# Kernel tuning notes

Measured on AMD Instinct MI355X. Metric: run time of the kernel, lower is better.

Reference implementation:

```python
import jax, jax.numpy as jnp
import numpy as np


def setup_inputs() -> dict:
    key = jax.random.key(0)
    k_cb, k_mask, k_y, k_yt, k_ym = jax.random.split(key, 5)
    B, L, M = 8, 2048, 4096
    CB = jax.random.normal(k_cb, (B, L, 3), dtype=jnp.float32) * 10.0
    # residue validity mask: mostly valid, some padding
    mask = (jax.random.uniform(k_mask, (B, L)) > 0.1).astype(jnp.float32)
    Y = jax.random.normal(k_y, (B, M, 3), dtype=jnp.float32) * 10.0
    Y_t = jax.random.randint(k_yt, (B, M), 0, 64, dtype=jnp.int32)
    Y_m = jax.random.randint(k_ym, (B, M), 0, 2, dtype=jnp.int32)
    return {"CB": CB, "mask": mask, "Y": Y, "Y_t": Y_t, "Y_m": Y_m,
            "number_of_ligand_atoms": 25}


def reference(CB, mask, Y, Y_t, Y_m, number_of_ligand_atoms):
    # CB: [B, L, 3], mask: [B, L], Y: [B, M, 3], Y_t/Y_m: [B, M]
    B, L, _ = CB.shape
    k = number_of_ligand_atoms
    Y_m_f = Y_m.astype(jnp.float32)
    mask_CBY = mask[:, :, None] * Y_m_f[:, None, :]          # [B, L, M]
    d = CB[:, :, None, :] - Y[:, None, :, :]                 # [B, L, M, 3]
    L2_AB = jnp.sum(d * d, axis=-1)                          # [B, L, M]
    L2_AB = L2_AB * mask_CBY + (1.0 - mask_CBY) * 1000.0
    # k smallest distances per (b, l); torch uses full argsort + slice,
    # top_k of the negated matrix selects the same set.
    neg_vals, nn_idx = jax.lax.top_k(-L2_AB, k)              # [B, L, k]
    L2_AB_nn = -neg_vals
    D_AB_closest = jnp.sqrt(L2_AB_nn[:, :, 0])               # [B, L]
    b_idx = jnp.arange(B)[:, None, None]                     # [B, 1, 1]
    Y_out = Y[b_idx, nn_idx]                                 # [B, L, k, 3]
    Y_t_out = Y_t[b_idx, nn_idx].astype(jnp.int32)           # [B, L, k]
    Y_m_out = Y_m[b_idx, nn_idx].astype(jnp.int32)           # [B, L, k]
    return Y_out, Y_t_out, Y_m_out, D_AB_closest
```

## Files before the change

### kernel.cpp

```cpp
#include <hip/hip_runtime.h>

#pragma clang fp contract(off)

typedef unsigned long long u64;
typedef unsigned int u32;
typedef unsigned short u16;
typedef float f32x2 __attribute__((ext_vector_type(2)));

#define BB 8
#define LL 2048
#define MM 4096
#define KK 25
#define WPB 16
#define TPB 1024
#define CAP 3072
#define SENT  0xFFFFFFFFFFFFFFFFull
#define SENTH 0xFFFFFFFFu

static __device__ __forceinline__ u32 wave_min_u32(u32 x) {
    u32 t;
    t = (u32)__builtin_amdgcn_update_dpp(0, (int)x, 0xB1, 0xF, 0xF, true);
    x = t < x ? t : x;
    t = (u32)__builtin_amdgcn_update_dpp(0, (int)x, 0x4E, 0xF, 0xF, true);
    x = t < x ? t : x;
    t = (u32)__builtin_amdgcn_update_dpp(0, (int)x, 0x141, 0xF, 0xF, true);
    x = t < x ? t : x;
    t = (u32)__builtin_amdgcn_update_dpp(0, (int)x, 0x140, 0xF, 0xF, true);
    x = t < x ? t : x;
    t = (u32)__builtin_amdgcn_update_dpp((int)x, (int)x, 0x142, 0xF, 0xF, false);
    x = t < x ? t : x;
    t = (u32)__builtin_amdgcn_update_dpp((int)x, (int)x, 0x143, 0xF, 0xF, false);
    x = t < x ? t : x;
    return (u32)__builtin_amdgcn_readlane((int)x, 63);
}

__global__ void __launch_bounds__(TPB, 8) knn_kernel(
    const float* __restrict__ CB, const float* __restrict__ maskA,
    const float* __restrict__ Y, const int* __restrict__ Yt,
    const int* __restrict__ Ym, float* __restrict__ out)
{
    __shared__ __align__(16) float sX[CAP];
    __shared__ __align__(16) float sY[CAP];
    __shared__ __align__(16) float sZ[CAP];
    __shared__ u16 sP16[CAP];
    __shared__ u16 sMidx[64];
    __shared__ int sWinc[16];
    __shared__ int sWbase[16];
    __shared__ int sVtot;
    __shared__ u32 sWinV[WPB][KK];
    __shared__ u16 sWinS[WPB][KK];

    const int tid  = threadIdx.x;
    const int lane = tid & 63;
    const int wv   = tid >> 6;
    const int blk  = blockIdx.x;
    const int b    = blk >> 7;
    const int qg   = blk & 127;

    const float* Yb  = Y  + (size_t)b * MM * 3;
    const int*   Ymb = Ym + (size_t)b * MM;
    const int*   Ytb = Yt + (size_t)b * MM;

    const int p0 = tid << 2;
    const float4 f0 = *(const float4*)(Yb + 3 * p0);
    const float4 f1 = *(const float4*)(Yb + 3 * p0 + 4);
    const float4 f2 = *(const float4*)(Yb + 3 * p0 + 8);
    const int4   m4 = *(const int4*)(Ymb + p0);
    const int v0 = (m4.x != 0), v1 = (m4.y != 0), v2 = (m4.z != 0), v3 = (m4.w != 0);
    const int cnt = v0 + v1 + v2 + v3;

    int inc = cnt;
#pragma unroll
    for (int off = 1; off < 64; off <<= 1) {
        const int t = __shfl_up(inc, off, 64);
        if (lane >= off) inc += t;
    }
    if (lane == 63) sWinc[wv] = inc;
    __syncthreads();
    if (tid < 16) {
        const int x = sWinc[tid];
        int ix = x;
#pragma unroll
        for (int off = 1; off < 16; off <<= 1) {
            const int t = __shfl_up(ix, off, 16);
            if (tid >= off) ix += t;
        }
        sWbase[tid] = ix - x;
        if (tid == 15) sVtot = ix;
    }
    __syncthreads();

    {
        int bs = sWbase[wv] + inc - cnt;
        int mb = p0 - bs;
        if (v0) { sX[bs]=f0.x; sY[bs]=f0.y; sZ[bs]=f0.z; sP16[bs]=(u16)(p0+0); bs++; }
        else    { if (mb < 64) sMidx[mb] = (u16)(p0 + 0); mb++; }
        if (v1) { sX[bs]=f0.w; sY[bs]=f1.x; sZ[bs]=f1.y; sP16[bs]=(u16)(p0+1); bs++; }
        else    { if (mb < 64) sMidx[mb] = (u16)(p0 + 1); mb++; }
        if (v2) { sX[bs]=f1.z; sY[bs]=f1.w; sZ[bs]=f2.x; sP16[bs]=(u16)(p0+2); bs++; }
        else    { if (mb < 64) sMidx[mb] = (u16)(p0 + 2); mb++; }
        if (v3) { sX[bs]=f2.y; sY[bs]=f2.z; sZ[bs]=f2.w; sP16[bs]=(u16)(p0+3); bs++; }
        else    { if (mb < 64) sMidx[mb] = (u16)(p0 + 3); mb++; }
    }
    const int V  = sVtot;
    const int NJ = (V + 127) >> 7;
    for (int c = V + tid; c < (NJ << 7); c += TPB) {
        sX[c] = __builtin_inff(); sY[c] = 0.0f; sZ[c] = 0.0f; sP16[c] = 4095;
    }
    __syncthreads();

    const int l = qg * WPB + wv;
    const int q = b * LL + l;

    float* out_y = out;
    float* out_t = out + (size_t)BB * LL * KK * 3;
    float* out_m = out_t + (size_t)BB * LL * KK;
    float* out_d = out_m + (size_t)BB * LL * KK;

    if (maskA[q] == 0.0f) {
        if (lane < KK) {
            const int p = lane;
            const size_t o = (size_t)q * KK + lane;
            out_y[3 * o + 0] = Yb[3 * p + 0];
            out_y[3 * o + 1] = Yb[3 * p + 1];
            out_y[3 * o + 2] = Yb[3 * p + 2];
            out_t[o] = (float)Ytb[p];
            out_m[o] = (float)Ymb[p];
            if (lane == 0) out_d[q] = sqrtf(1000.0f);
        }
        return;
    }

    const float cx = CB[3 * q + 0];
    const float cy = CB[3 * q + 1];
    const float cz = CB[3 * q + 2];

    float v1f = 3.0e38f, v2f = 3.0e38f, v3f = 3.0e38f, v4f = 3.0e38f;
    u32 J = 0u;
    const u32 SEL1 = 0x06050400u;
    const u32 SEL2 = 0x06050004u;
    const u32 SEL3 = 0x06000504u;
    const u32 SEL4 = 0x00060504u;
    auto ins = [&](float v, u32 id) {
        const bool c1 = v < v1f, c2 = v < v2f, c3 = v < v3f, c4 = v < v4f;
        const u32 sel = c1 ? SEL1 : (c2 ? SEL2 : (c3 ? SEL3 : SEL4));
        const u32 Jp  = __builtin_amdgcn_perm(J, id, sel);
        const float n2 = __builtin_amdgcn_fmed3f(v, v1f, v2f);
        const float n3 = __builtin_amdgcn_fmed3f(v, v2f, v3f);
        const float n4 = __builtin_amdgcn_fmed3f(v, v3f, v4f);
        v1f = fminf(v, v1f);
        v2f = n2; v3f = n3; v4f = n4;
        J = c4 ? Jp : J;
    };

    const f32x2 cxx = {cx, cx}, cyy = {cy, cy}, czz = {cz, cz};
#pragma unroll 4
    for (int j = 0; j < NJ; ++j) {
        const int base = (j << 7) + (lane << 1);
        const f32x2 xp = *(const f32x2*)&sX[base];
        const f32x2 yp = *(const f32x2*)&sY[base];
        const f32x2 zp = *(const f32x2*)&sZ[base];
        const f32x2 dx = cxx - xp;
        const f32x2 dy = cyy - yp;
        const f32x2 dz = czz - zp;
        const f32x2 dsq = (dx * dx + dy * dy) + dz * dz;
        ins(dsq.x, (u32)(j << 1));
        ins(dsq.y, (u32)((j << 1) | 1));
    }

    auto slotof = [&](u32 id) -> u32 {
        return ((id >> 1) << 7) | (u32)(lane << 1) | (id & 1u);
    };

    u32 h1 = __float_as_uint(v1f) + 1u;
    u32 h2 = __float_as_uint(v2f) + 1u;
    u32 h3 = __float_as_uint(v3f) + 1u;
    u32 h4 = __float_as_uint(v4f) + 1u;
    u64 lref = ((u64)h4 << 32) | slotof((J >> 24) & 0xFFu);

#pragma unroll 1
    for (int it = 0; it < KK; ++it) {
        if (it >= 4 && __any(h1 == SENTH)) {
            const bool need = (h1 == SENTH);
            u64 found = SENT;
            const int NI = NJ << 1;
#pragma unroll 4
            for (int id = 0; id < NI; ++id) {
                const u32 s = slotof((u32)id);
                const float dx = cx - sX[s];
                const float dy = cy - sY[s];
                const float dz = cz - sZ[s];
                const float v = (dx * dx + dy * dy) + dz * dz;
                const u64 key = ((u64)(__float_as_uint(v) + 1u) << 32) | s;
                if (key > lref && key < found) found = key;
            }
            if (need) {
                const u32 s = (u32)found & 0xFFFFu;
                h1 = (u32)(found >> 32);
                J = (J & ~0xFFu) | (((s >> 7) << 1) | (s & 1u));
                lref = found;
            }
        }
        const u32 bv = wave_min_u32(h1);
        const u64 ball = __ballot(h1 == bv);
        bool win = (h1 == bv);
        if (__popcll(ball) != 1) {
            const u32 vl = slotof(J & 0xFFu);
            u32 cp = win ? vl : 0xFFFFFFFFu;
#pragma unroll
            for (int off = 32; off; off >>= 1) {
                const u32 o = __shfl_xor(cp, off, 64);
                cp = (o < cp) ? o : cp;
            }
            win = win && (vl == cp);
        }
        if (win) {
            sWinV[wv][it] = h1;
            sWinS[wv][it] = (u16)slotof(J & 0xFFu);
            h1 = h2; h2 = h3; h3 = h4; h4 = SENTH;
            J >>= 8;
        }
    }

    u32 mvh = 0; u32 mslot = 0;
    if (lane < KK) { mvh = sWinV[wv][lane]; mslot = sWinS[wv][lane]; }
    const bool less = (lane < KK) && (mvh < 0x447A0001u);
    const int nless = __popcll(__ballot(less));
    if (lane < KK) {
        int p; float val, mflag;
        if (lane < nless) {
            p = (int)sP16[mslot];
            val = __uint_as_float(mvh - 1u);
            mflag = 1.0f;
        } else {
            p = (int)sMidx[lane - nless];
            val = 1000.0f;
            mflag = 0.0f;
        }
        const size_t o = (size_t)q * KK + lane;
        out_y[3 * o + 0] = Yb[3 * p + 0];
        out_y[3 * o + 1] = Yb[3 * p + 1];
        out_y[3 * o + 2] = Yb[3 * p + 2];
        out_t[o] = (float)Ytb[p];
        out_m[o] = mflag;
        if (lane == 0) out_d[q] = sqrtf(val);
    }
}

extern "C" void kernel_launch(void* const* d_in, const int* in_sizes, int n_in,
                              void* d_out, int out_size, void* d_ws, size_t ws_size,
                              hipStream_t stream) {
    const float* CB   = (const float*)d_in[0];
    const float* mask = (const float*)d_in[1];
    const float* Y    = (const float*)d_in[2];
    const int*   Yt   = (const int*)d_in[3];
    const int*   Ym   = (const int*)d_in[4];
    float* out = (float*)d_out;

    dim3 grid(BB * LL / WPB);
    dim3 block(TPB);
    hipLaunchKernelGGL(knn_kernel, grid, block, 0, stream, CB, mask, Y, Yt, Ym, out);
}
```

Baseline: 105.4 us.

## Replace serial 25-round wave-min extraction with bitonic-sort threshold selection

Instead of running 25 sequential wave-wide min reductions to pick the k nearest candidates, the kernel bitonic-sorts each lane's best value across the wave to get a threshold, compacts all per-lane candidates at or below it into shared memory, and bitonic-sorts those 64 keys to read off the top 25 directly. A validity check (candidate count exceeding 64, or some lane's 4-deep list possibly being exhausted before the 25th key) falls back to the original iterative path. This is meant to cut the long serial chain of reductions and shuffles per query. In exchange it adds two full 64-lane sorting networks, one of them on 64-bit keys, plus a prefix scan and extra shared memory traffic.

```diff
diff --git a/kernel.cpp b/kernel.cpp
--- a/kernel.cpp
+++ b/kernel.cpp
@@ -32,6 +32,38 @@
     t = (u32)__builtin_amdgcn_update_dpp((int)x, (int)x, 0x143, 0xF, 0xF, false);
     x = t < x ? t : x;
     return (u32)__builtin_amdgcn_readlane((int)x, 63);
+}
+
+static __device__ __forceinline__ u32 sort64_u32(u32 key, int lane) {
+#pragma unroll
+    for (int k = 2; k <= 64; k <<= 1) {
+#pragma unroll
+        for (int j = k >> 1; j >= 1; j >>= 1) {
+            const u32 o = (u32)__shfl_xor((int)key, j, 64);
+            const bool takeMin = ((lane & k) == 0) == ((lane & j) == 0);
+            const u32 mn = o < key ? o : key;
+            const u32 mx = o < key ? key : o;
+            key = takeMin ? mn : mx;
+        }
+    }
+    return key;
+}
+
+static __device__ __forceinline__ u64 sort64_u64(u64 key, int lane) {
+#pragma unroll
+    for (int k = 2; k <= 64; k <<= 1) {
+#pragma unroll
+        for (int j = k >> 1; j >= 1; j >>= 1) {
+            const u32 olo = (u32)__shfl_xor((int)(u32)key, j, 64);
+            const u32 ohi = (u32)__shfl_xor((int)(u32)(key >> 32), j, 64);
+            const u64 o = ((u64)ohi << 32) | olo;
+            const bool takeMin = ((lane & k) == 0) == ((lane & j) == 0);
+            const u64 mn = o < key ? o : key;
+            const u64 mx = o < key ? key : o;
+            key = takeMin ? mn : mx;
+        }
+    }
+    return key;
 }
 
 __global__ void __launch_bounds__(TPB, 8) knn_kernel(
@@ -47,8 +79,7 @@
     __shared__ int sWinc[16];
     __shared__ int sWbase[16];
     __shared__ int sVtot;
-    __shared__ u32 sWinV[WPB][KK];
-    __shared__ u16 sWinS[WPB][KK];
+    __shared__ u64 sExt[WPB][64];
 
     const int tid  = threadIdx.x;
     const int lane = tid & 63;
@@ -67,9 +98,9 @@
     const float4 f2 = *(const float4*)(Yb + 3 * p0 + 8);
     const int4   m4 = *(const int4*)(Ymb + p0);
     const int v0 = (m4.x != 0), v1 = (m4.y != 0), v2 = (m4.z != 0), v3 = (m4.w != 0);
-    const int cnt = v0 + v1 + v2 + v3;
-
-    int inc = cnt;
+    const int cnt0 = v0 + v1 + v2 + v3;
+
+    int inc = cnt0;
 #pragma unroll
     for (int off = 1; off < 64; off <<= 1) {
         const int t = __shfl_up(inc, off, 64);
@@ -91,7 +122,7 @@
     __syncthreads();
 
     {
-        int bs = sWbase[wv] + inc - cnt;
+        int bs = sWbase[wv] + inc - cnt0;
         int mb = p0 - bs;
         if (v0) { sX[bs]=f0.x; sY[bs]=f0.y; sZ[bs]=f0.z; sP16[bs]=(u16)(p0+0); bs++; }
         else    { if (mb < 64) sMidx[mb] = (u16)(p0 + 0); mb++; }
@@ -172,58 +203,95 @@
         return ((id >> 1) << 7) | (u32)(lane << 1) | (id & 1u);
     };
 
+    const u32 s1 = slotof( J        & 0xFFu);
+    const u32 s2 = slotof((J >>  8) & 0xFFu);
+    const u32 s3 = slotof((J >> 16) & 0xFFu);
+    const u32 s4 = slotof((J >> 24) & 0xFFu);
     u32 h1 = __float_as_uint(v1f) + 1u;
     u32 h2 = __float_as_uint(v2f) + 1u;
     u32 h3 = __float_as_uint(v3f) + 1u;
     u32 h4 = __float_as_uint(v4f) + 1u;
-    u64 lref = ((u64)h4 << 32) | slotof((J >> 24) & 0xFFu);
-
+    u64 lref = ((u64)h4 << 32) | s4;
+
+    bool fb = false;
+    u64 myk = 0;
+    {
+        const u32 T = (u32)__builtin_amdgcn_readlane((int)sort64_u32(h1, lane), 24);
+        const int c1 = (h1 <= T), c2 = (h2 <= T), c3 = (h3 <= T), c4 = (h4 <= T);
+        const int cnt = c1 + c2 + c3 + c4;
+        int incl = cnt;
+#pragma unroll
+        for (int off = 1; off < 64; off <<= 1) {
+            const int t = __shfl_up(incl, off, 64);
+            if (lane >= off) incl += t;
+        }
+        const int total = __builtin_amdgcn_readlane(incl, 63);
+        if (total > 64) {
+            fb = true;
+        } else {
+            u64* sE = sExt[wv];
+            sE[lane] = SENT;
+            int pos = incl - cnt;
+            if (c1) { sE[pos] = ((u64)h1 << 32) | s1; pos++; }
+            if (c2) { sE[pos] = ((u64)h2 << 32) | s2; pos++; }
+            if (c3) { sE[pos] = ((u64)h3 << 32) | s3; pos++; }
+            if (c4) { sE[pos] = ((u64)h4 << 32) | s4; pos++; }
+            myk = sort64_u64(sE[lane], lane);
+            const u32 k25lo = (u32)__builtin_amdgcn_readlane((int)(u32)myk, 24);
+            const u32 k25hi = (u32)__builtin_amdgcn_readlane((int)(u32)(myk >> 32), 24);
+            const u64 K25 = ((u64)k25hi << 32) | k25lo;
+            if (__any(lref < K25)) fb = true;
+        }
+    }
+
+    if (fb) {
 #pragma unroll 1
-    for (int it = 0; it < KK; ++it) {
-        if (it >= 4 && __any(h1 == SENTH)) {
-            const bool need = (h1 == SENTH);
-            u64 found = SENT;
-            const int NI = NJ << 1;
+        for (int it = 0; it < KK; ++it) {
+            if (it >= 4 && __any(h1 == SENTH)) {
+                const bool need = (h1 == SENTH);
+                u64 found = SENT;
+                const int NI = NJ << 1;
 #pragma unroll 4
-            for (int id = 0; id < NI; ++id) {
-                const u32 s = slotof((u32)id);
-                const float dx = cx - sX[s];
-                const float dy = cy - sY[s];
-                const float dz = cz - sZ[s];
-                const float v = (dx * dx + dy * dy) + dz * dz;
-                const u64 key = ((u64)(__float_as_uint(v) + 1u) << 32) | s;
-                if (key > lref && key < found) found = key;
+                for (int id = 0; id < NI; ++id) {
+                    const u32 s = slotof((u32)id);
+                    const float dx = cx - sX[s];
+                    const float dy = cy - sY[s];
+                    const float dz = cz - sZ[s];
+                    const float v = (dx * dx + dy * dy) + dz * dz;
+                    const u64 key = ((u64)(__float_as_uint(v) + 1u) << 32) | s;
+                    if (key > lref && key < found) found = key;
+                }
+                if (need) {
+                    const u32 s = (u32)found & 0xFFFFu;
+                    h1 = (u32)(found >> 32);
+                    J = (J & ~0xFFu) | (((s >> 7) << 1) | (s & 1u));
+                    lref = found;
+                }
             }
-            if (need) {
-                const u32 s = (u32)found & 0xFFFFu;
-                h1 = (u32)(found >> 32);
-                J = (J & ~0xFFu) | (((s >> 7) << 1) | (s & 1u));
-                lref = found;
+            const u32 bv = wave_min_u32(h1);
+            const u64 ball = __ballot(h1 == bv);
+            bool win = (h1 == bv);
+            if (__popcll(ball) != 1) {
+                const u32 vl = slotof(J & 0xFFu);
+                u32 cp = win ? vl : 0xFFFFFFFFu;
+#pragma unroll
+                for (int off = 32; off; off >>= 1) {
+                    const u32 o = __shfl_xor(cp, off, 64);
+                    cp = (o < cp) ? o : cp;
+                }
+                win = win && (vl == cp);
             }
-        }
-        const u32 bv = wave_min_u32(h1);
-        const u64 ball = __ballot(h1 == bv);
-        bool win = (h1 == bv);
-        if (__popcll(ball) != 1) {
-            const u32 vl = slotof(J & 0xFFu);
-            u32 cp = win ? vl : 0xFFFFFFFFu;
-#pragma unroll
-            for (int off = 32; off; off >>= 1) {
-                const u32 o = __shfl_xor(cp, off, 64);
-                cp = (o < cp) ? o : cp;
+            if (win) {
+                sExt[wv][it] = ((u64)h1 << 32) | slotof(J & 0xFFu);
+                h1 = h2; h2 = h3; h3 = h4; h4 = SENTH;
+                J >>= 8;
             }
-            win = win && (vl == cp);
-        }
-        if (win) {
-            sWinV[wv][it] = h1;
-            sWinS[wv][it] = (u16)slotof(J & 0xFFu);
-            h1 = h2; h2 = h3; h3 = h4; h4 = SENTH;
-            J >>= 8;
-        }
-    }
-
-    u32 mvh = 0; u32 mslot = 0;
-    if (lane < KK) { mvh = sWinV[wv][lane]; mslot = sWinS[wv][lane]; }
+        }
+        if (lane < KK) myk = sExt[wv][lane];
+    }
+
+    const u32 mvh   = (u32)(myk >> 32);
+    const u32 mslot = (u32)myk & 0xFFFFu;
     const bool less = (lane < KK) && (mvh < 0x447A0001u);
     const int nless = __popcll(__ballot(less));
     if (lane < KK) {
```

New measurement: 107.6 us. 1.02x slower.

## Replace serial 25-round wave selection with threshold-filtered rank sort fast path

Applied to the files above, without the earlier changes.

Each lane now scans 4 consecutive candidates per iteration using float4 LDS loads, which halves the number of iterations. After the scan, a fast path takes the wave-wide minimum of each lane's 4th-best value as a threshold and compacts all candidates at or below it into shared memory. It then rank-sorts them in parallel to pick the top 25, replacing the 25 serial wave-min/ballot rounds. If more than 64 candidates qualify, or if any lane's local list may be missing a needed element, it falls back to the old iterative path.

```diff
diff --git a/kernel.cpp b/kernel.cpp
--- a/kernel.cpp
+++ b/kernel.cpp
@@ -47,8 +47,8 @@
     __shared__ int sWinc[16];
     __shared__ int sWbase[16];
     __shared__ int sVtot;
-    __shared__ u32 sWinV[WPB][KK];
-    __shared__ u16 sWinS[WPB][KK];
+    __shared__ u64 sExt[WPB][64];
+    __shared__ u64 sR[WPB][KK];
 
     const int tid  = threadIdx.x;
     const int lane = tid & 63;
@@ -67,9 +67,9 @@
     const float4 f2 = *(const float4*)(Yb + 3 * p0 + 8);
     const int4   m4 = *(const int4*)(Ymb + p0);
     const int v0 = (m4.x != 0), v1 = (m4.y != 0), v2 = (m4.z != 0), v3 = (m4.w != 0);
-    const int cnt = v0 + v1 + v2 + v3;
-
-    int inc = cnt;
+    const int cnt0 = v0 + v1 + v2 + v3;
+
+    int inc = cnt0;
 #pragma unroll
     for (int off = 1; off < 64; off <<= 1) {
         const int t = __shfl_up(inc, off, 64);
@@ -91,7 +91,7 @@
     __syncthreads();
 
     {
-        int bs = sWbase[wv] + inc - cnt;
+        int bs = sWbase[wv] + inc - cnt0;
         int mb = p0 - bs;
         if (v0) { sX[bs]=f0.x; sY[bs]=f0.y; sZ[bs]=f0.z; sP16[bs]=(u16)(p0+0); bs++; }
         else    { if (mb < 64) sMidx[mb] = (u16)(p0 + 0); mb++; }
@@ -103,8 +103,8 @@
         else    { if (mb < 64) sMidx[mb] = (u16)(p0 + 3); mb++; }
     }
     const int V  = sVtot;
-    const int NJ = (V + 127) >> 7;
-    for (int c = V + tid; c < (NJ << 7); c += TPB) {
+    const int NJ = (V + 255) >> 8;
+    for (int c = V + tid; c < (NJ << 8); c += TPB) {
         sX[c] = __builtin_inff(); sY[c] = 0.0f; sZ[c] = 0.0f; sP16[c] = 4095;
     }
     __syncthreads();
@@ -154,76 +154,125 @@
     };
 
     const f32x2 cxx = {cx, cx}, cyy = {cy, cy}, czz = {cz, cz};
-#pragma unroll 4
+#pragma unroll 2
     for (int j = 0; j < NJ; ++j) {
-        const int base = (j << 7) + (lane << 1);
-        const f32x2 xp = *(const f32x2*)&sX[base];
-        const f32x2 yp = *(const f32x2*)&sY[base];
-        const f32x2 zp = *(const f32x2*)&sZ[base];
-        const f32x2 dx = cxx - xp;
-        const f32x2 dy = cyy - yp;
-        const f32x2 dz = czz - zp;
-        const f32x2 dsq = (dx * dx + dy * dy) + dz * dz;
-        ins(dsq.x, (u32)(j << 1));
-        ins(dsq.y, (u32)((j << 1) | 1));
+        const int base = (j << 8) + (lane << 2);
+        const float4 xq = *(const float4*)&sX[base];
+        const float4 yq = *(const float4*)&sY[base];
+        const float4 zq = *(const float4*)&sZ[base];
+        f32x2 dx = cxx - f32x2{xq.x, xq.y};
+        f32x2 dy = cyy - f32x2{yq.x, yq.y};
+        f32x2 dz = czz - f32x2{zq.x, zq.y};
+        const f32x2 d01 = (dx * dx + dy * dy) + dz * dz;
+        dx = cxx - f32x2{xq.z, xq.w};
+        dy = cyy - f32x2{yq.z, yq.w};
+        dz = czz - f32x2{zq.z, zq.w};
+        const f32x2 d23 = (dx * dx + dy * dy) + dz * dz;
+        ins(d01.x, (u32)(j << 2));
+        ins(d01.y, (u32)((j << 2) | 1));
+        ins(d23.x, (u32)((j << 2) | 2));
+        ins(d23.y, (u32)((j << 2) | 3));
     }
 
     auto slotof = [&](u32 id) -> u32 {
-        return ((id >> 1) << 7) | (u32)(lane << 1) | (id & 1u);
+        return ((id >> 2) << 8) | (u32)(lane << 2) | (id & 3u);
     };
 
+    const u32 s1 = slotof( J        & 0xFFu);
+    const u32 s2 = slotof((J >>  8) & 0xFFu);
+    const u32 s3 = slotof((J >> 16) & 0xFFu);
+    const u32 s4 = slotof((J >> 24) & 0xFFu);
     u32 h1 = __float_as_uint(v1f) + 1u;
     u32 h2 = __float_as_uint(v2f) + 1u;
     u32 h3 = __float_as_uint(v3f) + 1u;
     u32 h4 = __float_as_uint(v4f) + 1u;
-    u64 lref = ((u64)h4 << 32) | slotof((J >> 24) & 0xFFu);
-
+    u64 lref = ((u64)h4 << 32) | s4;
+
+    bool fb = false;
+    u64 myk = 0;
+    {
+        const u32 T = wave_min_u32(h4);
+        const bool c1 = (h1 <= T), c2 = (h2 <= T), c3 = (h3 <= T), c4 = (h4 <= T);
+        const u64 b1 = __ballot(c1), b2 = __ballot(c2);
+        const u64 b3 = __ballot(c3), b4 = __ballot(c4);
+        const int n1 = __popcll(b1), n2 = __popcll(b2), n3 = __popcll(b3);
+        const int total = n1 + n2 + n3 + __popcll(b4);
+        if (total > 64) {
+            fb = true;
+        } else {
+            const u64 below = (1ull << lane) - 1ull;
+            u64* sE = sExt[wv];
+            sE[lane] = SENT;
+            if (lane == 24) sR[wv][24] = SENT;
+            int pos = __popcll(b1 & below);
+            if (c1) sE[pos] = ((u64)h1 << 32) | s1;
+            pos = n1 + __popcll(b2 & below);
+            if (c2) sE[pos] = ((u64)h2 << 32) | s2;
+            pos = n1 + n2 + __popcll(b3 & below);
+            if (c3) sE[pos] = ((u64)h3 << 32) | s3;
+            pos = n1 + n2 + n3 + __popcll(b4 & below);
+            if (c4) sE[pos] = ((u64)h4 << 32) | s4;
+            const u64 mk = sE[lane];
+            int rank = 0;
+            const int tot = (total + 7) & ~7;
+#pragma unroll 8
+            for (int i = 0; i < tot; ++i)
+                rank += (sE[i] < mk) ? 1 : 0;
+            if (rank < KK && mk != SENT) sR[wv][rank] = mk;
+            const u64 K25 = sR[wv][24];
+            if (__any(lref < K25)) fb = true;
+            else if (lane < KK) myk = sR[wv][lane];
+        }
+    }
+
+    if (fb) {
 #pragma unroll 1
-    for (int it = 0; it < KK; ++it) {
-        if (it >= 4 && __any(h1 == SENTH)) {
-            const bool need = (h1 == SENTH);
-            u64 found = SENT;
-            const int NI = NJ << 1;
+        for (int it = 0; it < KK; ++it) {
+            if (it >= 4 && __any(h1 == SENTH)) {
+                const bool need = (h1 == SENTH);
+                u64 found = SENT;
+                const int NI = NJ << 2;
 #pragma unroll 4
-            for (int id = 0; id < NI; ++id) {
-                const u32 s = slotof((u32)id);
-                const float dx = cx - sX[s];
-                const float dy = cy - sY[s];
-                const float dz = cz - sZ[s];
-                const float v = (dx * dx + dy * dy) + dz * dz;
-                const u64 key = ((u64)(__float_as_uint(v) + 1u) << 32) | s;
-                if (key > lref && key < found) found = key;
+                for (int id = 0; id < NI; ++id) {
+                    const u32 s = slotof((u32)id);
+                    const float dx = cx - sX[s];
+                    const float dy = cy - sY[s];
+                    const float dz = cz - sZ[s];
+                    const float v = (dx * dx + dy * dy) + dz * dz;
+                    const u64 key = ((u64)(__float_as_uint(v) + 1u) << 32) | s;
+                    if (key > lref && key < found) found = key;
+                }
+                if (need) {
+                    const u32 s = (u32)found & 0xFFFFu;
+                    h1 = (u32)(found >> 32);
+                    J = (J & ~0xFFu) | (((s >> 8) << 2) | (s & 3u));
+                    lref = found;
+                }
             }
-            if (need) {
-                const u32 s = (u32)found & 0xFFFFu;
-                h1 = (u32)(found >> 32);
-                J = (J & ~0xFFu) | (((s >> 7) << 1) | (s & 1u));
-                lref = found;
+            const u32 bv = wave_min_u32(h1);
+            const u64 ball = __ballot(h1 == bv);
+            bool win = (h1 == bv);
+            if (__popcll(ball) != 1) {
+                const u32 vl = slotof(J & 0xFFu);
+                u32 cp = win ? vl : 0xFFFFFFFFu;
+#pragma unroll
+                for (int off = 32; off; off >>= 1) {
+                    const u32 o = __shfl_xor(cp, off, 64);
+                    cp = (o < cp) ? o : cp;
+                }
+                win = win && (vl == cp);
             }
-        }
-        const u32 bv = wave_min_u32(h1);
-        const u64 ball = __ballot(h1 == bv);
-        bool win = (h1 == bv);
-        if (__popcll(ball) != 1) {
-            const u32 vl = slotof(J & 0xFFu);
-            u32 cp = win ? vl : 0xFFFFFFFFu;
-#pragma unroll
-            for (int off = 32; off; off >>= 1) {
-                const u32 o = __shfl_xor(cp, off, 64);
-                cp = (o < cp) ? o : cp;
+            if (win) {
+                sExt[wv][it] = ((u64)h1 << 32) | slotof(J & 0xFFu);
+                h1 = h2; h2 = h3; h3 = h4; h4 = SENTH;
+                J >>= 8;
             }
-            win = win && (vl == cp);
-        }
-        if (win) {
-            sWinV[wv][it] = h1;
-            sWinS[wv][it] = (u16)slotof(J & 0xFFu);
-            h1 = h2; h2 = h3; h3 = h4; h4 = SENTH;
-            J >>= 8;
-        }
-    }
-
-    u32 mvh = 0; u32 mslot = 0;
-    if (lane < KK) { mvh = sWinV[wv][lane]; mslot = sWinS[wv][lane]; }
+        }
+        if (lane < KK) myk = sExt[wv][lane];
+    }
+
+    const u32 mvh   = (u32)(myk >> 32);
+    const u32 mslot = (u32)myk & 0xFFFFu;
     const bool less = (lane < KK) && (mvh < 0x447A0001u);
     const int nless = __popcll(__ballot(less));
     if (lane < KK) {
```

Measured after the change: 103.7 us. About the same (-1.7%).
